# Kernel tuning notes

Measured on AMD Instinct MI355X. Metric: run time of the kernel, lower is better.

Reference implementation:

```python
import jax, jax.numpy as jnp
import numpy as np

HIDDEN = 128
N_LAYERS = 6
N_NODES = 50000
N_EDGES = 640000


def _glorot(key, shape):
    fan_in, fan_out = shape[0], shape[1]
    lim = (6.0 / (fan_in + fan_out)) ** 0.5
    return jax.random.uniform(key, shape, jnp.float32, -lim, lim)


def setup_inputs() -> dict:
    key = jax.random.key(0)
    ks = jax.random.split(key, 8)
    pos = jax.random.normal(ks[0], (N_NODES, 3), jnp.float32)
    edge_attr = jax.random.normal(ks[1], (N_EDGES, 3), jnp.float32)
    edge_index = jax.random.randint(ks[2], (2, N_EDGES), 0, N_NODES, jnp.int64)
    enc_w = _glorot(ks[3], (3, HIDDEN)); enc_b = jnp.zeros((HIDDEN,), jnp.float32)
    dec_w = _glorot(ks[4], (HIDDEN, 3)); dec_b = jnp.zeros((3,), jnp.float32)
    lk = jax.random.split(ks[5], 4 * N_LAYERS)
    edge_w1 = jnp.stack([_glorot(lk[4 * i + 0], (3 * HIDDEN, HIDDEN)) for i in range(N_LAYERS)])
    edge_w2 = jnp.stack([_glorot(lk[4 * i + 1], (HIDDEN, HIDDEN)) for i in range(N_LAYERS)])
    node_w1 = jnp.stack([_glorot(lk[4 * i + 2], (2 * HIDDEN, HIDDEN)) for i in range(N_LAYERS)])
    node_w2 = jnp.stack([_glorot(lk[4 * i + 3], (HIDDEN, HIDDEN)) for i in range(N_LAYERS)])
    edge_b1 = jnp.zeros((N_LAYERS, HIDDEN), jnp.float32)
    edge_b2 = jnp.zeros((N_LAYERS, HIDDEN), jnp.float32)
    node_b1 = jnp.zeros((N_LAYERS, HIDDEN), jnp.float32)
    node_b2 = jnp.zeros((N_LAYERS, HIDDEN), jnp.float32)
    return dict(pos=pos, edge_attr=edge_attr, edge_index=edge_index,
                enc_w=enc_w, enc_b=enc_b, dec_w=dec_w, dec_b=dec_b,
                edge_w1=edge_w1, edge_b1=edge_b1, edge_w2=edge_w2, edge_b2=edge_b2,
                node_w1=node_w1, node_b1=node_b1, node_w2=node_w2, node_b2=node_b2)


def _interaction(x, ef, src, dst, ew1, eb1, ew2, eb2, nw1, nb1, nw2, nb2, n_nodes):
    # message: concat(x_i=x[dst], x_j=x[src], edge_feature) -> edge MLP
    m = jnp.concatenate([x[dst], x[src], ef], axis=-1)            # [E, 3H]
    m = jax.nn.relu(m @ ew1 + eb1) @ ew2 + eb2                     # [E, H]
    # scatter-mean by target node
    sums = jax.ops.segment_sum(m, dst, num_segments=n_nodes)      # [N, H]
    cnt = jax.ops.segment_sum(jnp.ones((m.shape[0],), m.dtype), dst, num_segments=n_nodes)
    aggr = sums / jnp.maximum(cnt, 1.0)[:, None]
    node = jnp.concatenate([x, aggr], axis=-1)                     # [N, 2H]
    node = jax.nn.relu(node @ nw1 + nb1) @ nw2 + nb2               # [N, H]
    return x + node, ef + m


def reference(pos, edge_attr, edge_index, enc_w, enc_b, dec_w, dec_b,
              edge_w1, edge_b1, edge_w2, edge_b2,
              node_w1, node_b1, node_w2, node_b2):
    n_nodes = pos.shape[0]
    src = edge_index[0]
    dst = edge_index[1]
    x = jnp.zeros((n_nodes, HIDDEN), jnp.float32)
    ef = edge_attr @ enc_w + enc_b
    for i in range(N_LAYERS):
        x, ef = _interaction(x, ef, src, dst,
                             edge_w1[i], edge_b1[i], edge_w2[i], edge_b2[i],
                             node_w1[i], node_b1[i], node_w2[i], node_b2[i], n_nodes)
    out = x @ dec_w + dec_b                                        # [N, 3]
    # F.normalize(dim=1, eps=1e-12)
    norm = jnp.linalg.norm(out, axis=1, keepdims=True)
    return out / jnp.maximum(norm, 1e-12)
```

## Files before the change

kernel.cpp:

```cpp
#include <hip/hip_runtime.h>
#include <cstdint>

#define HIDDEN  128
#define NLAYERS 6
#define NNODES  50000
#define NEDGES  640000

typedef short short8 __attribute__((ext_vector_type(8)));
typedef float f32x4  __attribute__((ext_vector_type(4)));

__device__ __forceinline__ float bf2f(unsigned short u) {
    return __uint_as_float(((unsigned int)u) << 16);
}
__device__ __forceinline__ unsigned short f2bf(float f) {
    unsigned int u = __float_as_uint(f);
    unsigned int r = u + 0x7FFFu + ((u >> 16) & 1u);
    return (unsigned short)(r >> 16);
}
__device__ __forceinline__ unsigned int pack2(float a, float b) {
    return (unsigned int)f2bf(a) | ((unsigned int)f2bf(b) << 16);
}
__device__ __forceinline__ void unpack8(uint4 v, float* f) {
    f[0] = bf2f((unsigned short)(v.x & 0xffff)); f[1] = bf2f((unsigned short)(v.x >> 16));
    f[2] = bf2f((unsigned short)(v.y & 0xffff)); f[3] = bf2f((unsigned short)(v.y >> 16));
    f[4] = bf2f((unsigned short)(v.z & 0xffff)); f[5] = bf2f((unsigned short)(v.z >> 16));
    f[6] = bf2f((unsigned short)(v.w & 0xffff)); f[7] = bf2f((unsigned short)(v.w >> 16));
}

__device__ __forceinline__ void barrier_lgkm() {
    asm volatile("s_waitcnt lgkmcnt(0)" ::: "memory");
    __builtin_amdgcn_s_barrier();
    __builtin_amdgcn_sched_barrier(0);
}

__global__ void detect_kernel(const int* __restrict__ ei, int* __restrict__ flag)
{
    int lane = threadIdx.x;
    int v = ei[2 * lane + 1];
    unsigned long long b = __ballot(v != 0);
    if (lane == 0) *flag = (b != 0ULL) ? 1 : 0;
}

__global__ void normidx_kernel(const int* __restrict__ ei, const int* __restrict__ flag,
                               int* __restrict__ s32, int* __restrict__ d32)
{
    int e = blockIdx.x * blockDim.x + threadIdx.x;
    if (e >= NEDGES) return;
    int s, d;
    if (*flag) { s = ei[e]; d = ei[NEDGES + e]; }
    else       { s = ei[2 * e]; d = ei[2 * (NEDGES + e)]; }
    s32[e] = min(max(s, 0), NNODES - 1);
    d32[e] = min(max(d, 0), NNODES - 1);
}

__global__ void degree_kernel(const int* __restrict__ dst, int* __restrict__ deg)
{
    int e = blockIdx.x * blockDim.x + threadIdx.x;
    if (e < NEDGES) atomicAdd(&deg[dst[e]], 1);
}

#define SCAN_T 1024
__global__ void scan_kernel(const int* __restrict__ deg, int* __restrict__ off,
                            int* __restrict__ cursor)
{
    __shared__ int part[SCAN_T];
    const int t = threadIdx.x;
    const int CH = (NNODES + SCAN_T - 1) / SCAN_T;
    const int base = t * CH;
    int s = 0;
    for (int i = 0; i < CH; ++i) {
        int idx = base + i;
        if (idx < NNODES) s += deg[idx];
    }
    part[t] = s;
    __syncthreads();
    for (int d = 1; d < SCAN_T; d <<= 1) {
        int v = (t >= d) ? part[t - d] : 0;
        __syncthreads();
        part[t] += v;
        __syncthreads();
    }
    int run = (t == 0) ? 0 : part[t - 1];
    for (int i = 0; i < CH; ++i) {
        int idx = base + i;
        if (idx < NNODES) {
            off[idx] = run;
            cursor[idx] = run;
            run += deg[idx];
        }
    }
    if (t == SCAN_T - 1) off[NNODES] = run;
}

__global__ void scatter_kernel(const int* __restrict__ s32, const int* __restrict__ d32,
                               int* __restrict__ cursor,
                               int* __restrict__ sp, int* __restrict__ dp, int* __restrict__ ep)
{
    int e = blockIdx.x * blockDim.x + threadIdx.x;
    if (e >= NEDGES) return;
    int d = d32[e];
    int p = atomicAdd(&cursor[d], 1);
    sp[p] = s32[e];
    dp[p] = d;
    ep[p] = e;
}

__global__ void transpose_kernel(const float* __restrict__ W, unsigned short* __restrict__ WT,
                                 int K, int N, int L)
{
    long idx = (long)blockIdx.x * 256 + threadIdx.x;
    long tot = (long)L * K * N;
    if (idx >= tot) return;
    int kn = (int)(idx % ((long)K * N));
    int l  = (int)(idx / ((long)K * N));
    int k = kn / N;
    int n = kn % N;
    WT[(long)l * K * N + (long)n * K + k] = f2bf(W[idx]);
}

__global__ void encode_kernel(const float* __restrict__ ea,
                              const float* __restrict__ w,
                              const float* __restrict__ b,
                              const int* __restrict__ ep,
                              unsigned short* __restrict__ ef)
{
    int idx = blockIdx.x * blockDim.x + threadIdx.x;
    int p = idx >> 5;
    if (p >= NEDGES) return;
    int e = ep[p];
    int j = (idx & 31) << 2;
    float a0 = ea[e * 3 + 0], a1 = ea[e * 3 + 1], a2 = ea[e * 3 + 2];
    float4 w0 = *(const float4*)(w + 0 * HIDDEN + j);
    float4 w1 = *(const float4*)(w + 1 * HIDDEN + j);
    float4 w2 = *(const float4*)(w + 2 * HIDDEN + j);
    float4 bb = *(const float4*)(b + j);
    ushort4 o;
    o.x = f2bf(fmaf(a0, w0.x, fmaf(a1, w1.x, fmaf(a2, w2.x, bb.x))));
    o.y = f2bf(fmaf(a0, w0.y, fmaf(a1, w1.y, fmaf(a2, w2.y, bb.y))));
    o.z = f2bf(fmaf(a0, w0.z, fmaf(a1, w1.z, fmaf(a2, w2.z, bb.z))));
    o.w = f2bf(fmaf(a0, w0.w, fmaf(a1, w1.w, fmaf(a2, w2.w, bb.w))));
    *(ushort4*)(ef + (long)p * HIDDEN + j) = o;
}

__global__ __launch_bounds__(256, 3)
void edge_layer_mfma(const unsigned short* __restrict__ Xa,
                     const unsigned short* __restrict__ Xb,
                     unsigned short* __restrict__ ef,
                     float* __restrict__ sums,
                     const int* __restrict__ sp,
                     const int* __restrict__ dp,
                     const unsigned short* __restrict__ W1T,
                     const float* __restrict__ b1,
                     const unsigned short* __restrict__ W2T,
                     const float* __restrict__ b2)
{
    __shared__ __align__(16) unsigned char buf[45056];
    unsigned short* As = (unsigned short*)buf;
    unsigned short* Hs = (unsigned short*)buf;
    unsigned short* Bs = (unsigned short*)(buf + 34816);
    __shared__ int dv[128];
    __shared__ int sv[128];

    const int tid = threadIdx.x;
    const long eb = (long)blockIdx.x * 128;
    if (tid < 128) dv[tid]       = dp[eb + tid];
    else           sv[tid - 128] = sp[eb + tid - 128];

    const int lane = tid & 63;
    const int wv   = tid >> 6;
    const int mn   = lane & 15;
    const int q    = lane >> 4;
    const int rr   = tid >> 1;
    const int o    = (tid & 1) << 4;
    const int bn   = tid >> 1;
    const int bk   = (tid & 1) << 4;

    f32x4 acc[2][8];
#pragma unroll
    for (int h = 0; h < 2; ++h)
#pragma unroll
        for (int t = 0; t < 8; ++t) acc[h][t] = (f32x4)0.0f;

    short8 efold0[4], efold1[4];

    uint4 pa0, pa1, pw0, pw1;
    {
        const unsigned short* epp = ef + (eb + rr) * HIDDEN + o;
        pa0 = *(const uint4*)epp;
        pa1 = *(const uint4*)(epp + 8);
        const unsigned short* wp = W1T + (long)bn * 384 + 256 + bk;
        pw0 = *(const uint4*)wp;
        pw1 = *(const uint4*)(wp + 8);
    }

    for (int c = 0; c < 4; ++c) {
        *(uint4*)&As[rr * 40 + o]      = pa0;
        *(uint4*)&As[rr * 40 + o + 8]  = pa1;
        *(uint4*)&Bs[bn * 40 + bk]     = pw0;
        *(uint4*)&Bs[bn * 40 + bk + 8] = pw1;
        barrier_lgkm();

        if (c + 1 < 4) {
            const int cn = c + 1;
            const unsigned short* epp = ef + (eb + rr) * HIDDEN + (cn << 5) + o;
            pa0 = *(const uint4*)epp;
            pa1 = *(const uint4*)(epp + 8);
            const unsigned short* wp = W1T + (long)bn * 384 + 256 + (cn << 5) + bk;
            pw0 = *(const uint4*)wp;
            pw1 = *(const uint4*)(wp + 8);
        }

        short8 af0 = *(short8*)&As[(wv * 32 + mn) * 40 + (q << 3)];
        short8 af1 = *(short8*)&As[(wv * 32 + 16 + mn) * 40 + (q << 3)];
        efold0[c] = af0;
        efold1[c] = af1;
#pragma unroll
        for (int nt = 0; nt < 8; ++nt) {
            short8 bf = *(short8*)&Bs[(nt * 16 + mn) * 40 + (q << 3)];
            acc[0][nt] = __builtin_amdgcn_mfma_f32_16x16x32_bf16(af0, bf, acc[0][nt], 0, 0, 0);
            acc[1][nt] = __builtin_amdgcn_mfma_f32_16x16x32_bf16(af1, bf, acc[1][nt], 0, 0, 0);
        }
        barrier_lgkm();
    }

#pragma unroll
    for (int h = 0; h < 2; ++h)
#pragma unroll
        for (int nt = 0; nt < 8; ++nt)
#pragma unroll
            for (int r = 0; r < 4; ++r)
                Hs[(wv * 32 + h * 16 + q * 4 + r) * 136 + nt * 16 + mn] = f2bf(acc[h][nt][r]);

    {
        const int row  = wv * 32 + (lane >> 1);
        const int ch   = (lane & 1) << 6;
        const unsigned short* xap = Xa + (long)dv[row] * HIDDEN + ch;
        const unsigned short* xbp = Xb + (long)sv[row] * HIDDEN + ch;
        unsigned short* hp = &Hs[row * 136 + ch];
#pragma unroll
        for (int i = 0; i < 8; ++i) {
            uint4 va = *(const uint4*)(xap + (i << 3));
            uint4 vb = *(const uint4*)(xbp + (i << 3));
            uint4 vp = *(uint4*)(hp + (i << 3));
            float fa[8], fb[8], fp[8];
            unpack8(va, fa); unpack8(vb, fb); unpack8(vp, fp);
            const float* bp = b1 + ch + (i << 3);
            uint4 nw;
            float h0 = fmaxf(fp[0] + fa[0] + fb[0] + bp[0], 0.0f);
            float h1 = fmaxf(fp[1] + fa[1] + fb[1] + bp[1], 0.0f);
            float h2 = fmaxf(fp[2] + fa[2] + fb[2] + bp[2], 0.0f);
            float h3 = fmaxf(fp[3] + fa[3] + fb[3] + bp[3], 0.0f);
            float h4 = fmaxf(fp[4] + fa[4] + fb[4] + bp[4], 0.0f);
            float h5 = fmaxf(fp[5] + fa[5] + fb[5] + bp[5], 0.0f);
            float h6 = fmaxf(fp[6] + fa[6] + fb[6] + bp[6], 0.0f);
            float h7 = fmaxf(fp[7] + fa[7] + fb[7] + bp[7], 0.0f);
            nw.x = pack2(h0, h1); nw.y = pack2(h2, h3);
            nw.z = pack2(h4, h5); nw.w = pack2(h6, h7);
            *(uint4*)(hp + (i << 3)) = nw;
        }
    }

    f32x4 acc2[2][8];
#pragma unroll
    for (int h = 0; h < 2; ++h)
#pragma unroll
        for (int t = 0; t < 8; ++t) acc2[h][t] = (f32x4)0.0f;
    {
        const unsigned short* wp = W2T + (long)bn * 128 + bk;
        pw0 = *(const uint4*)wp;
        pw1 = *(const uint4*)(wp + 8);
    }
    for (int c = 0; c < 4; ++c) {
        *(uint4*)&Bs[bn * 40 + bk]     = pw0;
        *(uint4*)&Bs[bn * 40 + bk + 8] = pw1;
        barrier_lgkm();
        if (c + 1 < 4) {
            const unsigned short* wp = W2T + (long)bn * 128 + ((c + 1) << 5) + bk;
            pw0 = *(const uint4*)wp;
            pw1 = *(const uint4*)(wp + 8);
        }
        short8 af0 = *(short8*)&Hs[(wv * 32 + mn) * 136 + (c << 5) + (q << 3)];
        short8 af1 = *(short8*)&Hs[(wv * 32 + 16 + mn) * 136 + (c << 5) + (q << 3)];
#pragma unroll
        for (int nt = 0; nt < 8; ++nt) {
            short8 bf = *(short8*)&Bs[(nt * 16 + mn) * 40 + (q << 3)];
            acc2[0][nt] = __builtin_amdgcn_mfma_f32_16x16x32_bf16(af0, bf, acc2[0][nt], 0, 0, 0);
            acc2[1][nt] = __builtin_amdgcn_mfma_f32_16x16x32_bf16(af1, bf, acc2[1][nt], 0, 0, 0);
        }
        barrier_lgkm();
    }

#pragma unroll
    for (int h = 0; h < 2; ++h)
#pragma unroll
        for (int nt = 0; nt < 8; ++nt) {
            float b2v = b2[nt * 16 + mn];
#pragma unroll
            for (int r = 0; r < 4; ++r)
                Hs[(wv * 32 + h * 16 + q * 4 + r) * 136 + nt * 16 + mn] = f2bf(acc2[h][nt][r] + b2v);
        }

#pragma unroll
    for (int h = 0; h < 2; ++h) {
        const int row = wv * 32 + h * 16 + mn;
        unsigned short* ep_ = ef + (eb + row) * HIDDEN + (q << 3);
#pragma unroll
        for (int c = 0; c < 4; ++c) {
            uint4 mh = *(uint4*)&Hs[row * 136 + (c << 5) + (q << 3)];
            float m[8], e[8];
            unpack8(mh, m);
            short8 eo = h ? efold1[c] : efold0[c];
            uint4 eu = *(uint4*)&eo;
            unpack8(eu, e);
            uint4 nw;
            nw.x = pack2(e[0] + m[0], e[1] + m[1]);
            nw.y = pack2(e[2] + m[2], e[3] + m[3]);
            nw.z = pack2(e[4] + m[4], e[5] + m[5]);
            nw.w = pack2(e[6] + m[6], e[7] + m[7]);
            *(uint4*)(ep_ + (c << 5)) = nw;
        }
    }

    {
        const int cp = (tid & 63) << 1;
        const int qr = tid >> 6;
        float s0 = 0.0f, s1 = 0.0f;
        int cur = dv[qr * 32];
        for (int r = 0; r < 32; ++r) {
            const int row = qr * 32 + r;
            const int d = dv[row];
            if (d != cur) {
                atomicAdd(&sums[(long)cur * HIDDEN + cp], s0);
                atomicAdd(&sums[(long)cur * HIDDEN + cp + 1], s1);
                s0 = 0.0f; s1 = 0.0f;
                cur = d;
            }
            unsigned int u = *(unsigned int*)&Hs[row * 136 + cp];
            s0 += bf2f((unsigned short)(u & 0xffff));
            s1 += bf2f((unsigned short)(u >> 16));
        }
        atomicAdd(&sums[(long)cur * HIDDEN + cp], s0);
        atomicAdd(&sums[(long)cur * HIDDEN + cp + 1], s1);
    }
}

__global__ __launch_bounds__(256, 5)
void node_layer_mfma(float* __restrict__ x,
                     float* __restrict__ sums,
                     const int* __restrict__ deg,
                     const unsigned short* __restrict__ N1T,
                     const float* __restrict__ b1,
                     const unsigned short* __restrict__ N2T,
                     const float* __restrict__ b2,
                     const unsigned short* __restrict__ W1Tn,
                     unsigned short* __restrict__ Xa,
                     unsigned short* __restrict__ Xb)
{
    __shared__ __align__(16) unsigned char nbuf[27648];
    unsigned short* As = (unsigned short*)nbuf;
    unsigned short* Hs = (unsigned short*)nbuf;
    unsigned short* Bs = (unsigned short*)(nbuf + 17408);
    __shared__ float cInv[64];

    const int tid = threadIdx.x;
    const long n0 = (long)blockIdx.x * 64;
    if (tid < 64) {
        long n = n0 + tid;
        cInv[tid] = (n < NNODES) ? 1.0f / fmaxf((float)deg[n], 1.0f) : 0.0f;
    }

    const int lane = tid & 63;
    const int wv   = tid >> 6;
    const int mn   = lane & 15;
    const int q    = lane >> 4;
    const int srow = tid >> 2;
    const int sseg = tid & 3;
    const int bn   = tid >> 1;
    const int bk   = (tid & 1) << 4;

    long nr = n0 + srow;
    if (nr >= NNODES) nr = NNODES - 1;

    barrier_lgkm();

    f32x4 acc[8];
#pragma unroll
    for (int t = 0; t < 8; ++t) acc[t] = (f32x4)0.0f;

    float4 pa0, pa1;
    uint4 pb0, pb1;
    {
        const float* spx = x + nr * HIDDEN + (sseg << 3);
        pa0 = *(const float4*)spx;
        pa1 = *(const float4*)(spx + 4);
        const unsigned short* wp = N1T + (long)bn * 256 + bk;
        pb0 = *(const uint4*)wp;
        pb1 = *(const uint4*)(wp + 8);
    }
    float scCur = 1.0f;
    for (int c = 0; c < 8; ++c) {
        {
            uint4 w;
            w.x = pack2(pa0.x * scCur, pa0.y * scCur); w.y = pack2(pa0.z * scCur, pa0.w * scCur);
            w.z = pack2(pa1.x * scCur, pa1.y * scCur); w.w = pack2(pa1.z * scCur, pa1.w * scCur);
            *(uint4*)&As[srow * 40 + (sseg << 3)] = w;
        }
        *(uint4*)&Bs[bn * 40 + bk]     = pb0;
        *(uint4*)&Bs[bn * 40 + bk + 8] = pb1;
        barrier_lgkm();
        if (c + 1 < 8) {
            const int cn = c + 1;
            const float* base = (cn < 4) ? x : sums;
            scCur = (cn < 4) ? 1.0f : cInv[srow];
            const float* spx = base + nr * HIDDEN + ((cn & 3) << 5) + (sseg << 3);
            pa0 = *(const float4*)spx;
            pa1 = *(const float4*)(spx + 4);
            const unsigned short* wp = N1T + (long)bn * 256 + (cn << 5) + bk;
            pb0 = *(const uint4*)wp;
            pb1 = *(const uint4*)(wp + 8);
        }
        short8 af = *(short8*)&As[(wv * 16 + mn) * 40 + (q << 3)];
#pragma unroll
        for (int nt = 0; nt < 8; ++nt) {
            short8 bf = *(short8*)&Bs[(nt * 16 + mn) * 40 + (q << 3)];
            acc[nt] = __builtin_amdgcn_mfma_f32_16x16x32_bf16(af, bf, acc[nt], 0, 0, 0);
        }
        barrier_lgkm();
    }

    {
        long row = n0 + srow;
        if (row < NNODES) {
            float4 z = make_float4(0.f, 0.f, 0.f, 0.f);
            float* p = sums + row * HIDDEN + (sseg << 5);
#pragma unroll
            for (int i = 0; i < 8; ++i) ((float4*)p)[i] = z;
        }
    }

#pragma unroll
    for (int nt = 0; nt < 8; ++nt) {
        float b1v = b1[nt * 16 + mn];
#pragma unroll
        for (int r = 0; r < 4; ++r) {
            float hv = fmaxf(acc[nt][r] + b1v, 0.0f);
            Hs[(wv * 16 + q * 4 + r) * 136 + nt * 16 + mn] = f2bf(hv);
        }
    }

    f32x4 acc2[8];
#pragma unroll
    for (int t = 0; t < 8; ++t) acc2[t] = (f32x4)0.0f;
    {
        const unsigned short* wp = N2T + (long)bn * 128 + bk;
        pb0 = *(const uint4*)wp;
        pb1 = *(const uint4*)(wp + 8);
    }
    for (int c = 0; c < 4; ++c) {
        *(uint4*)&Bs[bn * 40 + bk]     = pb0;
        *(uint4*)&Bs[bn * 40 + bk + 8] = pb1;
        barrier_lgkm();
        if (c + 1 < 4) {
            const unsigned short* wp = N2T + (long)bn * 128 + ((c + 1) << 5) + bk;
            pb0 = *(const uint4*)wp;
            pb1 = *(const uint4*)(wp + 8);
        }
        short8 af = *(short8*)&Hs[(wv * 16 + mn) * 136 + (c << 5) + (q << 3)];
#pragma unroll
        for (int nt = 0; nt < 8; ++nt) {
            short8 bf = *(short8*)&Bs[(nt * 16 + mn) * 40 + (q << 3)];
            acc2[nt] = __builtin_amdgcn_mfma_f32_16x16x32_bf16(af, bf, acc2[nt], 0, 0, 0);
        }
        barrier_lgkm();
    }

#pragma unroll
    for (int nt = 0; nt < 8; ++nt) {
        float b2v = b2[nt * 16 + mn];
#pragma unroll
        for (int r = 0; r < 4; ++r) {
            long row = n0 + wv * 16 + q * 4 + r;
            float xn = 0.0f;
            if (row < NNODES) {
                float* p = x + row * HIDDEN + nt * 16 + mn;
                xn = *p + acc2[nt][r] + b2v;
                *p = xn;
            }
            Hs[(wv * 16 + q * 4 + r) * 136 + nt * 16 + mn] = f2bf(xn);
        }
    }

    if (W1Tn) {
#pragma unroll
        for (int half = 0; half < 2; ++half) {
            f32x4 accN[8];
#pragma unroll
            for (int t = 0; t < 8; ++t) accN[t] = (f32x4)0.0f;
            const int kbase = half << 7;
            {
                const unsigned short* wp = W1Tn + (long)bn * 384 + kbase + bk;
                pb0 = *(const uint4*)wp;
                pb1 = *(const uint4*)(wp + 8);
            }
            for (int c = 0; c < 4; ++c) {
                *(uint4*)&Bs[bn * 40 + bk]     = pb0;
                *(uint4*)&Bs[bn * 40 + bk + 8] = pb1;
                barrier_lgkm();
                if (c + 1 < 4) {
                    const unsigned short* wp = W1Tn + (long)bn * 384 + kbase + ((c + 1) << 5) + bk;
                    pb0 = *(const uint4*)wp;
                    pb1 = *(const uint4*)(wp + 8);
                }
                short8 af = *(short8*)&Hs[(wv * 16 + mn) * 136 + (c << 5) + (q << 3)];
#pragma unroll
                for (int nt = 0; nt < 8; ++nt) {
                    short8 bf = *(short8*)&Bs[(nt * 16 + mn) * 40 + (q << 3)];
                    accN[nt] = __builtin_amdgcn_mfma_f32_16x16x32_bf16(af, bf, accN[nt], 0, 0, 0);
                }
                barrier_lgkm();
            }
            unsigned short* Xout = half ? Xb : Xa;
#pragma unroll
            for (int nt = 0; nt < 8; ++nt) {
#pragma unroll
                for (int r = 0; r < 4; ++r) {
                    long row = n0 + wv * 16 + q * 4 + r;
                    if (row < NNODES) {
                        Xout[row * HIDDEN + nt * 16 + mn] = f2bf(accN[nt][r]);
                    }
                }
            }
        }
    }
}

__global__ void decode_kernel(const float* __restrict__ x,
                              const float* __restrict__ w,
                              const float* __restrict__ b,
                              float* __restrict__ out)
{
    int gid = blockIdx.x * blockDim.x + threadIdx.x;
    int node = gid >> 6;
    int lane = threadIdx.x & 63;
    if (node >= NNODES) return;
    float a0 = 0.f, a1 = 0.f, a2 = 0.f;
#pragma unroll
    for (int k = lane; k < HIDDEN; k += 64) {
        float xv = x[(long)node * HIDDEN + k];
        a0 = fmaf(xv, w[k * 3 + 0], a0);
        a1 = fmaf(xv, w[k * 3 + 1], a1);
        a2 = fmaf(xv, w[k * 3 + 2], a2);
    }
#pragma unroll
    for (int off = 32; off > 0; off >>= 1) {
        a0 += __shfl_down(a0, off);
        a1 += __shfl_down(a1, off);
        a2 += __shfl_down(a2, off);
    }
    if (lane == 0) {
        a0 += b[0]; a1 += b[1]; a2 += b[2];
        float nrm = sqrtf(a0 * a0 + a1 * a1 + a2 * a2);
        float inv = 1.0f / fmaxf(nrm, 1e-12f);
        out[(long)node * 3 + 0] = a0 * inv;
        out[(long)node * 3 + 1] = a1 * inv;
        out[(long)node * 3 + 2] = a2 * inv;
    }
}

extern "C" void kernel_launch(void* const* d_in, const int* in_sizes, int n_in,
                              void* d_out, int out_size, void* d_ws, size_t ws_size,
                              hipStream_t stream)
{
    const float* edge_attr = (const float*)d_in[1];
    const int*   ei        = (const int*)d_in[2];
    const float* enc_w     = (const float*)d_in[3];
    const float* enc_b     = (const float*)d_in[4];
    const float* dec_w     = (const float*)d_in[5];
    const float* dec_b     = (const float*)d_in[6];
    const float* edge_w1   = (const float*)d_in[7];
    const float* edge_b1   = (const float*)d_in[8];
    const float* edge_w2   = (const float*)d_in[9];
    const float* edge_b2   = (const float*)d_in[10];
    const float* node_w1   = (const float*)d_in[11];
    const float* node_b1   = (const float*)d_in[12];
    const float* node_w2   = (const float*)d_in[13];
    const float* node_b2   = (const float*)d_in[14];

    char* ws = (char*)d_ws;
    unsigned short* ef  = (unsigned short*)(ws);
    float* x      = (float*)(ws + 163840000L);
    float* sums   = (float*)(ws + 189440000L);
    int*   src32  = (int*)  (ws + 215040000L);
    int*   dst32  = (int*)  (ws + 217600000L);
    int*   sp     = (int*)  (ws + 220160000L);
    int*   dp     = (int*)  (ws + 222720000L);
    int*   eperm  = (int*)  (ws + 225280000L);
    int*   deg    = (int*)  (ws + 227840000L);
    int*   off    = (int*)  (ws + 228040704L);
    int*   cursor = (int*)  (ws + 228241408L);
    int*   flag   = (int*)  (ws + 228442112L);
    unsigned short* W1T = (unsigned short*)(ws + 228442176L);
    unsigned short* W2T = (unsigned short*)(ws + 229032000L);
    unsigned short* N1T = (unsigned short*)(ws + 229228608L);
    unsigned short* N2T = (unsigned short*)(ws + 229621824L);
    unsigned short* Xa  = (unsigned short*)(ws + 229818432L);
    unsigned short* Xb  = (unsigned short*)(ws + 242618432L);

    float* out = (float*)d_out;

    hipMemsetAsync(x, 0, (size_t)NNODES * HIDDEN * sizeof(float), stream);
    hipMemsetAsync(sums, 0, (size_t)NNODES * HIDDEN * sizeof(float), stream);
    hipMemsetAsync(deg, 0, 200704, stream);
    hipMemsetAsync(Xa, 0, 25600000, stream);

    detect_kernel<<<1, 64, 0, stream>>>(ei, flag);
    normidx_kernel<<<(NEDGES + 255) / 256, 256, 0, stream>>>(ei, flag, src32, dst32);
    degree_kernel<<<(NEDGES + 255) / 256, 256, 0, stream>>>(dst32, deg);
    scan_kernel<<<1, SCAN_T, 0, stream>>>(deg, off, cursor);
    scatter_kernel<<<(NEDGES + 255) / 256, 256, 0, stream>>>(src32, dst32, cursor, sp, dp, eperm);
    encode_kernel<<<(NEDGES * 32 + 255) / 256, 256, 0, stream>>>(edge_attr, enc_w, enc_b, eperm, ef);

    transpose_kernel<<<(6 * 384 * 128 + 255) / 256, 256, 0, stream>>>(edge_w1, W1T, 384, 128, 6);
    transpose_kernel<<<(6 * 128 * 128 + 255) / 256, 256, 0, stream>>>(edge_w2, W2T, 128, 128, 6);
    transpose_kernel<<<(6 * 256 * 128 + 255) / 256, 256, 0, stream>>>(node_w1, N1T, 256, 128, 6);
    transpose_kernel<<<(6 * 128 * 128 + 255) / 256, 256, 0, stream>>>(node_w2, N2T, 128, 128, 6);

    for (int l = 0; l < NLAYERS; ++l) {
        edge_layer_mfma<<<NEDGES / 128, 256, 0, stream>>>(
            Xa, Xb, ef, sums, sp, dp,
            W1T + (long)l * 384 * 128, edge_b1 + (long)l * HIDDEN,
            W2T + (long)l * 128 * 128, edge_b2 + (long)l * HIDDEN);
        const unsigned short* w1next = (l + 1 < NLAYERS) ? (W1T + (long)(l + 1) * 384 * 128) : nullptr;
        node_layer_mfma<<<(NNODES + 63) / 64, 256, 0, stream>>>(
            x, sums, deg,
            N1T + (long)l * 256 * 128, node_b1 + (long)l * HIDDEN,
            N2T + (long)l * 128 * 128, node_b2 + (long)l * HIDDEN,
            w1next, Xa, Xb);
    }

    decode_kernel<<<(NNODES * 64 + 255) / 256, 256, 0, stream>>>(x, dec_w, dec_b, out);
}
```

Measured before the change: 1.556 ms.

## Use hardware bf16 packing, nontemporal edge-feature traffic, and XCD-aware block remap

Replaces the software round-to-nearest bf16 conversion with the v_cvt_pk_bf16_f32 instruction, which converts two floats per instruction in all epilogues. Edge-feature loads and stores are made nontemporal so the streaming ef traffic does not evict the gathered node features from cache. It also remaps edge-layer block IDs across the 8 XCDs so neighbouring edge blocks land on the same die. Together these aim to cut conversion ALU work and cache pollution, at the cost of depending on the grid size being divisible by 8 and on hardware rounding that may differ slightly for NaN and edge cases.

```diff
diff --git a/kernel.cpp b/kernel.cpp
--- a/kernel.cpp
+++ b/kernel.cpp
@@ -8,6 +8,8 @@
 
 typedef short short8 __attribute__((ext_vector_type(8)));
 typedef float f32x4  __attribute__((ext_vector_type(4)));
+typedef unsigned int   u32x4 __attribute__((ext_vector_type(4)));
+typedef unsigned short u16x4 __attribute__((ext_vector_type(4)));
 
 __device__ __forceinline__ float bf2f(unsigned short u) {
     return __uint_as_float(((unsigned int)u) << 16);
@@ -18,9 +20,11 @@
     return (unsigned short)(r >> 16);
 }
 __device__ __forceinline__ unsigned int pack2(float a, float b) {
-    return (unsigned int)f2bf(a) | ((unsigned int)f2bf(b) << 16);
-}
-__device__ __forceinline__ void unpack8(uint4 v, float* f) {
+    unsigned int r;
+    asm("v_cvt_pk_bf16_f32 %0, %1, %2" : "=v"(r) : "v"(a), "v"(b));
+    return r;
+}
+__device__ __forceinline__ void unpack8u(u32x4 v, float* f) {
     f[0] = bf2f((unsigned short)(v.x & 0xffff)); f[1] = bf2f((unsigned short)(v.x >> 16));
     f[2] = bf2f((unsigned short)(v.y & 0xffff)); f[3] = bf2f((unsigned short)(v.y >> 16));
     f[4] = bf2f((unsigned short)(v.z & 0xffff)); f[5] = bf2f((unsigned short)(v.z >> 16));
@@ -134,12 +138,12 @@
     float4 w1 = *(const float4*)(w + 1 * HIDDEN + j);
     float4 w2 = *(const float4*)(w + 2 * HIDDEN + j);
     float4 bb = *(const float4*)(b + j);
-    ushort4 o;
+    u16x4 o;
     o.x = f2bf(fmaf(a0, w0.x, fmaf(a1, w1.x, fmaf(a2, w2.x, bb.x))));
     o.y = f2bf(fmaf(a0, w0.y, fmaf(a1, w1.y, fmaf(a2, w2.y, bb.y))));
     o.z = f2bf(fmaf(a0, w0.z, fmaf(a1, w1.z, fmaf(a2, w2.z, bb.z))));
     o.w = f2bf(fmaf(a0, w0.w, fmaf(a1, w1.w, fmaf(a2, w2.w, bb.w))));
-    *(ushort4*)(ef + (long)p * HIDDEN + j) = o;
+    __builtin_nontemporal_store(o, (u16x4*)(ef + (long)p * HIDDEN + j));
 }
 
 __global__ __launch_bounds__(256, 3)
@@ -162,7 +166,11 @@
     __shared__ int sv[128];
 
     const int tid = threadIdx.x;
-    const long eb = (long)blockIdx.x * 128;
+    const int nwg = (int)gridDim.x;
+    const int bid = (int)blockIdx.x;
+    const int sb  = (bid & 7) * (nwg >> 3) + (bid >> 3);
+    const long eb = (long)sb * 128;
+
     if (tid < 128) dv[tid]       = dp[eb + tid];
     else           sv[tid - 128] = sp[eb + tid - 128];
 
@@ -183,31 +191,31 @@
 
     short8 efold0[4], efold1[4];
 
-    uint4 pa0, pa1, pw0, pw1;
+    u32x4 pa0, pa1, pw0, pw1;
     {
         const unsigned short* epp = ef + (eb + rr) * HIDDEN + o;
-        pa0 = *(const uint4*)epp;
-        pa1 = *(const uint4*)(epp + 8);
+        pa0 = __builtin_nontemporal_load((const u32x4*)epp);
+        pa1 = __builtin_nontemporal_load((const u32x4*)(epp + 8));
         const unsigned short* wp = W1T + (long)bn * 384 + 256 + bk;
-        pw0 = *(const uint4*)wp;
-        pw1 = *(const uint4*)(wp + 8);
+        pw0 = *(const u32x4*)wp;
+        pw1 = *(const u32x4*)(wp + 8);
     }
 
     for (int c = 0; c < 4; ++c) {
-        *(uint4*)&As[rr * 40 + o]      = pa0;
-        *(uint4*)&As[rr * 40 + o + 8]  = pa1;
-        *(uint4*)&Bs[bn * 40 + bk]     = pw0;
-        *(uint4*)&Bs[bn * 40 + bk + 8] = pw1;
+        *(u32x4*)&As[rr * 40 + o]      = pa0;
+        *(u32x4*)&As[rr * 40 + o + 8]  = pa1;
+        *(u32x4*)&Bs[bn * 40 + bk]     = pw0;
+        *(u32x4*)&Bs[bn * 40 + bk + 8] = pw1;
         barrier_lgkm();
 
         if (c + 1 < 4) {
             const int cn = c + 1;
             const unsigned short* epp = ef + (eb + rr) * HIDDEN + (cn << 5) + o;
-            pa0 = *(const uint4*)epp;
-            pa1 = *(const uint4*)(epp + 8);
+            pa0 = __builtin_nontemporal_load((const u32x4*)epp);
+            pa1 = __builtin_nontemporal_load((const u32x4*)(epp + 8));
             const unsigned short* wp = W1T + (long)bn * 384 + 256 + (cn << 5) + bk;
-            pw0 = *(const uint4*)wp;
-            pw1 = *(const uint4*)(wp + 8);
+            pw0 = *(const u32x4*)wp;
+            pw1 = *(const u32x4*)(wp + 8);
         }
 
         short8 af0 = *(short8*)&As[(wv * 32 + mn) * 40 + (q << 3)];
@@ -228,8 +236,11 @@
 #pragma unroll
         for (int nt = 0; nt < 8; ++nt)
 #pragma unroll
-            for (int r = 0; r < 4; ++r)
-                Hs[(wv * 32 + h * 16 + q * 4 + r) * 136 + nt * 16 + mn] = f2bf(acc[h][nt][r]);
+            for (int r = 0; r < 4; r += 2) {
+                unsigned int p = pack2(acc[h][nt][r], acc[h][nt][r + 1]);
+                Hs[(wv * 32 + h * 16 + q * 4 + r)     * 136 + nt * 16 + mn] = (unsigned short)p;
+                Hs[(wv * 32 + h * 16 + q * 4 + r + 1) * 136 + nt * 16 + mn] = (unsigned short)(p >> 16);
+            }
 
     {
         const int row  = wv * 32 + (lane >> 1);
@@ -239,13 +250,13 @@
         unsigned short* hp = &Hs[row * 136 + ch];
 #pragma unroll
         for (int i = 0; i < 8; ++i) {
-            uint4 va = *(const uint4*)(xap + (i << 3));
-            uint4 vb = *(const uint4*)(xbp + (i << 3));
-            uint4 vp = *(uint4*)(hp + (i << 3));
+            u32x4 va = *(const u32x4*)(xap + (i << 3));
+            u32x4 vb = *(const u32x4*)(xbp + (i << 3));
+            u32x4 vp = *(u32x4*)(hp + (i << 3));
             float fa[8], fb[8], fp[8];
-            unpack8(va, fa); unpack8(vb, fb); unpack8(vp, fp);
+            unpack8u(va, fa); unpack8u(vb, fb); unpack8u(vp, fp);
             const float* bp = b1 + ch + (i << 3);
-            uint4 nw;
+            u32x4 nw;
             float h0 = fmaxf(fp[0] + fa[0] + fb[0] + bp[0], 0.0f);
             float h1 = fmaxf(fp[1] + fa[1] + fb[1] + bp[1], 0.0f);
             float h2 = fmaxf(fp[2] + fa[2] + fb[2] + bp[2], 0.0f);
@@ -256,7 +267,7 @@
             float h7 = fmaxf(fp[7] + fa[7] + fb[7] + bp[7], 0.0f);
             nw.x = pack2(h0, h1); nw.y = pack2(h2, h3);
             nw.z = pack2(h4, h5); nw.w = pack2(h6, h7);
-            *(uint4*)(hp + (i << 3)) = nw;
+            *(u32x4*)(hp + (i << 3)) = nw;
         }
     }
 
@@ -267,17 +278,17 @@
         for (int t = 0; t < 8; ++t) acc2[h][t] = (f32x4)0.0f;
     {
         const unsigned short* wp = W2T + (long)bn * 128 + bk;
-        pw0 = *(const uint4*)wp;
-        pw1 = *(const uint4*)(wp + 8);
+        pw0 = *(const u32x4*)wp;
+        pw1 = *(const u32x4*)(wp + 8);
     }
     for (int c = 0; c < 4; ++c) {
-        *(uint4*)&Bs[bn * 40 + bk]     = pw0;
-        *(uint4*)&Bs[bn * 40 + bk + 8] = pw1;
+        *(u32x4*)&Bs[bn * 40 + bk]     = pw0;
+        *(u32x4*)&Bs[bn * 40 + bk + 8] = pw1;
         barrier_lgkm();
         if (c + 1 < 4) {
             const unsigned short* wp = W2T + (long)bn * 128 + ((c + 1) << 5) + bk;
-            pw0 = *(const uint4*)wp;
-            pw1 = *(const uint4*)(wp + 8);
+            pw0 = *(const u32x4*)wp;
+            pw1 = *(const u32x4*)(wp + 8);
         }
         short8 af0 = *(short8*)&Hs[(wv * 32 + mn) * 136 + (c << 5) + (q << 3)];
         short8 af1 = *(short8*)&Hs[(wv * 32 + 16 + mn) * 136 + (c << 5) + (q << 3)];
@@ -296,8 +307,11 @@
         for (int nt = 0; nt < 8; ++nt) {
             float b2v = b2[nt * 16 + mn];
 #pragma unroll
-            for (int r = 0; r < 4; ++r)
-                Hs[(wv * 32 + h * 16 + q * 4 + r) * 136 + nt * 16 + mn] = f2bf(acc2[h][nt][r] + b2v);
+            for (int r = 0; r < 4; r += 2) {
+                unsigned int p = pack2(acc2[h][nt][r] + b2v, acc2[h][nt][r + 1] + b2v);
+                Hs[(wv * 32 + h * 16 + q * 4 + r)     * 136 + nt * 16 + mn] = (unsigned short)p;
+                Hs[(wv * 32 + h * 16 + q * 4 + r + 1) * 136 + nt * 16 + mn] = (unsigned short)(p >> 16);
+            }
         }
 
 #pragma unroll
@@ -306,18 +320,18 @@
         unsigned short* ep_ = ef + (eb + row) * HIDDEN + (q << 3);
 #pragma unroll
         for (int c = 0; c < 4; ++c) {
-            uint4 mh = *(uint4*)&Hs[row * 136 + (c << 5) + (q << 3)];
+            u32x4 mh = *(u32x4*)&Hs[row * 136 + (c << 5) + (q << 3)];
             float m[8], e[8];
-            unpack8(mh, m);
+            unpack8u(mh, m);
             short8 eo = h ? efold1[c] : efold0[c];
-            uint4 eu = *(uint4*)&eo;
-            unpack8(eu, e);
-            uint4 nw;
+            u32x4 eu = *(u32x4*)&eo;
+            unpack8u(eu, e);
+            u32x4 nw;
             nw.x = pack2(e[0] + m[0], e[1] + m[1]);
             nw.y = pack2(e[2] + m[2], e[3] + m[3]);
             nw.z = pack2(e[4] + m[4], e[5] + m[5]);
             nw.w = pack2(e[6] + m[6], e[7] + m[7]);
-            *(uint4*)(ep_ + (c << 5)) = nw;
+            __builtin_nontemporal_store(nw, (u32x4*)(ep_ + (c << 5)));
         }
     }
 
@@ -388,25 +402,25 @@
     for (int t = 0; t < 8; ++t) acc[t] = (f32x4)0.0f;
 
     float4 pa0, pa1;
-    uint4 pb0, pb1;
+    u32x4 pb0, pb1;
     {
         const float* spx = x + nr * HIDDEN + (sseg << 3);
         pa0 = *(const float4*)spx;
         pa1 = *(const float4*)(spx + 4);
         const unsigned short* wp = N1T + (long)bn * 256 + bk;
-        pb0 = *(const uint4*)wp;
-        pb1 = *(const uint4*)(wp + 8);
+        pb0 = *(const u32x4*)wp;
+        pb1 = *(const u32x4*)(wp + 8);
     }
     float scCur = 1.0f;
     for (int c = 0; c < 8; ++c) {
         {
-            uint4 w;
+            u32x4 w;
             w.x = pack2(pa0.x * scCur, pa0.y * scCur); w.y = pack2(pa0.z * scCur, pa0.w * scCur);
             w.z = pack2(pa1.x * scCur, pa1.y * scCur); w.w = pack2(pa1.z * scCur, pa1.w * scCur);
-            *(uint4*)&As[srow * 40 + (sseg << 3)] = w;
-        }
-        *(uint4*)&Bs[bn * 40 + bk]     = pb0;
-        *(uint4*)&Bs[bn * 40 + bk + 8] = pb1;
+            *(u32x4*)&As[srow * 40 + (sseg << 3)] = w;
+        }
+        *(u32x4*)&Bs[bn * 40 + bk]     = pb0;
+        *(u32x4*)&Bs[bn * 40 + bk + 8] = pb1;
         barrier_lgkm();
         if (c + 1 < 8) {
             const int cn = c + 1;
@@ -416,8 +430,8 @@
             pa0 = *(const float4*)spx;
             pa1 = *(const float4*)(spx + 4);
             const unsigned short* wp = N1T + (long)bn * 256 + (cn << 5) + bk;
-            pb0 = *(const uint4*)wp;
-            pb1 = *(const uint4*)(wp + 8);
+            pb0 = *(const u32x4*)wp;
+            pb1 = *(const u32x4*)(wp + 8);
         }
         short8 af = *(short8*)&As[(wv * 16 + mn) * 40 + (q << 3)];
 #pragma unroll
@@ -442,9 +456,12 @@
     for (int nt = 0; nt < 8; ++nt) {
         float b1v = b1[nt * 16 + mn];
 #pragma unroll
-        for (int r = 0; r < 4; ++r) {
-            float hv = fmaxf(acc[nt][r] + b1v, 0.0f);
-            Hs[(wv * 16 + q * 4 + r) * 136 + nt * 16 + mn] = f2bf(hv);
+        for (int r = 0; r < 4; r += 2) {
+            float h0 = fmaxf(acc[nt][r]     + b1v, 0.0f);
+            float h1 = fmaxf(acc[nt][r + 1] + b1v, 0.0f);
+            unsigned int p = pack2(h0, h1);
+            Hs[(wv * 16 + q * 4 + r)     * 136 + nt * 16 + mn] = (unsigned short)p;
+            Hs[(wv * 16 + q * 4 + r + 1) * 136 + nt * 16 + mn] = (unsigned short)(p >> 16);
         }
     }
 
@@ -453,17 +470,17 @@
     for (int t = 0; t < 8; ++t) acc2[t] = (f32x4)0.0f;
     {
         const unsigned short* wp = N2T + (long)bn * 128 + bk;
-        pb0 = *(const uint4*)wp;
-        pb1 = *(const uint4*)(wp + 8);
+        pb0 = *(const u32x4*)wp;
+        pb1 = *(const u32x4*)(wp + 8);
     }
     for (int c = 0; c < 4; ++c) {
-        *(uint4*)&Bs[bn * 40 + bk]     = pb0;
-        *(uint4*)&Bs[bn * 40 + bk + 8] = pb1;
+        *(u32x4*)&Bs[bn * 40 + bk]     = pb0;
+        *(u32x4*)&Bs[bn * 40 + bk + 8] = pb1;
         barrier_lgkm();
         if (c + 1 < 4) {
             const unsigned short* wp = N2T + (long)bn * 128 + ((c + 1) << 5) + bk;
-            pb0 = *(const uint4*)wp;
-            pb1 = *(const uint4*)(wp + 8);
+            pb0 = *(const u32x4*)wp;
+            pb1 = *(const u32x4*)(wp + 8);
         }
         short8 af = *(short8*)&Hs[(wv * 16 + mn) * 136 + (c << 5) + (q << 3)];
 #pragma unroll
@@ -477,6 +494,7 @@
 #pragma unroll
     for (int nt = 0; nt < 8; ++nt) {
         float b2v = b2[nt * 16 + mn];
+        float xns[4];
 #pragma unroll
         for (int r = 0; r < 4; ++r) {
             long row = n0 + wv * 16 + q * 4 + r;
@@ -486,8 +504,14 @@
                 xn = *p + acc2[nt][r] + b2v;
                 *p = xn;
             }
-            Hs[(wv * 16 + q * 4 + r) * 136 + nt * 16 + mn] = f2bf(xn);
-        }
+            xns[r] = xn;
+        }
+        unsigned int p0 = pack2(xns[0], xns[1]);
+        unsigned int p1 = pack2(xns[2], xns[3]);
+        Hs[(wv * 16 + q * 4 + 0) * 136 + nt * 16 + mn] = (unsigned short)p0;
+        Hs[(wv * 16 + q * 4 + 1) * 136 + nt * 16 + mn] = (unsigned short)(p0 >> 16);
+        Hs[(wv * 16 + q * 4 + 2) * 136 + nt * 16 + mn] = (unsigned short)p1;
+        Hs[(wv * 16 + q * 4 + 3) * 136 + nt * 16 + mn] = (unsigned short)(p1 >> 16);
     }
 
     if (W1Tn) {
@@ -499,17 +523,17 @@
             const int kbase = half << 7;
             {
                 const unsigned short* wp = W1Tn + (long)bn * 384 + kbase + bk;
-                pb0 = *(const uint4*)wp;
-                pb1 = *(const uint4*)(wp + 8);
+                pb0 = *(const u32x4*)wp;
+                pb1 = *(const u32x4*)(wp + 8);
             }
             for (int c = 0; c < 4; ++c) {
-                *(uint4*)&Bs[bn * 40 + bk]     = pb0;
-                *(uint4*)&Bs[bn * 40 + bk + 8] = pb1;
+                *(u32x4*)&Bs[bn * 40 + bk]     = pb0;
+                *(u32x4*)&Bs[bn * 40 + bk + 8] = pb1;
                 barrier_lgkm();
                 if (c + 1 < 4) {
                     const unsigned short* wp = W1Tn + (long)bn * 384 + kbase + ((c + 1) << 5) + bk;
-                    pb0 = *(const uint4*)wp;
-                    pb1 = *(const uint4*)(wp + 8);
+                    pb0 = *(const u32x4*)wp;
+                    pb1 = *(const u32x4*)(wp + 8);
                 }
                 short8 af = *(short8*)&Hs[(wv * 16 + mn) * 136 + (c << 5) + (q << 3)];
 #pragma unroll
@@ -523,11 +547,13 @@
 #pragma unroll
             for (int nt = 0; nt < 8; ++nt) {
 #pragma unroll
-                for (int r = 0; r < 4; ++r) {
-                    long row = n0 + wv * 16 + q * 4 + r;
-                    if (row < NNODES) {
-                        Xout[row * HIDDEN + nt * 16 + mn] = f2bf(accN[nt][r]);
-                    }
+                for (int r = 0; r < 4; r += 2) {
+                    unsigned int p = pack2(accN[nt][r], accN[nt][r + 1]);
+                    long row0 = n0 + wv * 16 + q * 4 + r;
+                    if (row0 < NNODES)
+                        Xout[row0 * HIDDEN + nt * 16 + mn] = (unsigned short)p;
+                    if (row0 + 1 < NNODES)
+                        Xout[(row0 + 1) * HIDDEN + nt * 16 + mn] = (unsigned short)(p >> 16);
                 }
             }
         }
```

Measured after the change: 1.870 ms. 1.2x slower.
